# Optimization experiments

Measured on AMD Instinct MI355X. Metric: run time of the kernel, lower is better.

The kernel has to match this reference:

```python
import jax, jax.numpy as jnp
import numpy as np

# Config matching init_kwargs / input shapes
DIM = 96        # dim == C
NH = 6          # num_heads
KS = 7          # kernel_size (local window)
GW = 4          # group_width for the grouped conv in Hadamard-attn branch
B, D, H, W = 2, 8, 96, 96
HD = DIM // NH          # head dim (dim_qk == dim_v == dim)
SCALE = HD ** -0.5      # qk_scale default: head_dim**-0.5
PAD = KS // 2
EPS = 1e-5


def setup_inputs() -> dict:
    key = jax.random.key(0)
    ks = jax.random.split(key, 10)
    s = 0.02
    return {
        "x": jax.random.normal(ks[0], (B, DIM, D, H, W), jnp.float32),
        # pre-norm LayerNorm params
        "ln_g": jnp.ones((DIM,), jnp.float32),
        "ln_b": jnp.zeros((DIM,), jnp.float32),
        # q,k projection (fused 1x1): out = 2*dim_qk
        "w_qk": s * jax.random.normal(ks[1], (2 * DIM, DIM), jnp.float32),
        "b_qk": jnp.zeros((2 * DIM,), jnp.float32),
        # v projection (1x1)
        "w_v": s * jax.random.normal(ks[2], (DIM, DIM), jnp.float32),
        "b_v": jnp.zeros((DIM,), jnp.float32),
        # Hadamard-attention branch: grouped KSxKS conv (groups = DIM//GW)
        "w_a1": s * jax.random.normal(ks[3], (DIM, GW, KS, KS), jnp.float32),
        "b_a1": jnp.zeros((DIM,), jnp.float32),
        # 1x1 conv producing per-head local attention logits (NH * KS^2 channels)
        "w_a2": s * jax.random.normal(ks[4], (NH * KS * KS, DIM), jnp.float32),
        "b_a2": jnp.zeros((NH * KS * KS,), jnp.float32),
        # ghost head (lam=1, gamma=1): attn = h_attn * ghost_mul + ghost_add
        "g_mul": 1.0 + s * jax.random.normal(ks[5], (NH * KS * KS,), jnp.float32),
        "g_add": s * jax.random.normal(ks[6], (NH * KS * KS,), jnp.float32),
        # output projection (1x1)
        "w_p": s * jax.random.normal(ks[7], (DIM, DIM), jnp.float32),
        "b_p": jnp.zeros((DIM,), jnp.float32),
    }


def _elsa_block(x, ln_g, ln_b, w_qk, b_qk, w_v, b_v, w_a1, b_a1, w_a2, b_a2,
                g_mul, g_add, w_p, b_p):
    """x: (Bp, H, W, C) channel-last frames. Pre-norm residual ELSA attention."""
    Bp, Hh, Ww, C = x.shape
    # LayerNorm over channels
    mu = jnp.mean(x, axis=-1, keepdims=True)
    var = jnp.mean(jnp.square(x - mu), axis=-1, keepdims=True)
    xn = (x - mu) * jax.lax.rsqrt(var + EPS) * ln_g + ln_b

    # 1x1 q,k,v projections (channel-last matmuls)
    qk = xn @ w_qk.T + b_qk                      # (Bp,H,W,2C)
    q, k = jnp.split(qk, 2, axis=-1)
    v = xn @ w_v.T + b_v                         # (Bp,H,W,C)

    # Hadamard product -> attention logits via grouped conv + GELU + 1x1
    h = jnp.transpose(q * k * SCALE, (0, 3, 1, 2))   # (Bp,C,H,W) NCHW
    a = jax.lax.conv_general_dilated(
        h, w_a1, window_strides=(1, 1), padding='SAME',
        feature_group_count=C // GW) + b_a1[None, :, None, None]
    a = jax.nn.gelu(a, approximate=False)
    a = jnp.einsum('bchw,oc->bohw', a, w_a2) + b_a2[None, :, None, None]

    # ghost head (lam=1, gamma=1): elementwise scale + static bias per (head, tap)
    attn = a * g_mul[None, :, None, None] + g_add[None, :, None, None]
    attn = attn.reshape(Bp, NH, KS * KS, Hh, Ww)     # (Bp,nh,k^2,H,W)

    # local window aggregation (unfold-free: 49 shifted fused multiply-adds)
    vr = jnp.transpose(v, (0, 3, 1, 2)).reshape(Bp, NH, HD, Hh, Ww)
    vp = jnp.pad(vr, ((0, 0), (0, 0), (0, 0), (PAD, PAD), (PAD, PAD)))
    out = jnp.zeros_like(vr)
    for i in range(KS):
        for j in range(KS):
            out = out + attn[:, :, i * KS + j, None] * vp[:, :, :, i:i + Hh, j:j + Ww]

    out = jnp.transpose(out.reshape(Bp, C, Hh, Ww), (0, 2, 3, 1))  # (Bp,H,W,C)
    y = out @ w_p.T + b_p
    return x + y


def reference(x, ln_g, ln_b, w_qk, b_qk, w_v, b_v, w_a1, b_a1, w_a2, b_a2,
              g_mul, g_add, w_p, b_p):
    b, c, d, hh, ww = x.shape
    # 'b c s h w -> (b s) h w c'
    xf = jnp.transpose(x, (0, 2, 3, 4, 1)).reshape(b * d, hh, ww, c)
    yf = _elsa_block(xf, ln_g, ln_b, w_qk, b_qk, w_v, b_v, w_a1, b_a1,
                     w_a2, b_a2, g_mul, g_add, w_p, b_p)
    # '(b s) h w c -> b c s h w'
    return jnp.transpose(yf.reshape(b, d, hh, ww, c), (0, 4, 1, 2, 3))
```

## Files before the change

### kernel.cpp

```cpp
#include <hip/hip_runtime.h>
#include <hip/hip_bf16.h>


typedef unsigned short u16;
typedef short bf16x8 __attribute__((ext_vector_type(8)));
typedef float floatx4 __attribute__((ext_vector_type(4)));
typedef unsigned short ushort8 __attribute__((ext_vector_type(8)));
typedef unsigned short ushort4v __attribute__((ext_vector_type(4)));
typedef unsigned int uint4v __attribute__((ext_vector_type(4)));
typedef unsigned int uint2v __attribute__((ext_vector_type(2)));
typedef _Float16 f16x2 __attribute__((ext_vector_type(2)));

#define PIX      9216
#define SCALE_QK 0.25f

__device__ __forceinline__ float lo2f(unsigned int u) {
  union { unsigned int i; float f; } z; z.i = u << 16; return z.f;
}
__device__ __forceinline__ float hi2f(unsigned int u) {
  union { unsigned int i; float f; } z; z.i = u & 0xFFFF0000u; return z.f;
}
__device__ __forceinline__ u16 f2b(float f) {
  union { float f; unsigned int i; } z; z.f = f;
  unsigned int r = z.i + 0x7fffu + ((z.i >> 16) & 1u);
  return (u16)(r >> 16);
}
__device__ __forceinline__ u16 f2h(float f) {
  _Float16 h = (_Float16)f;
  union { _Float16 h; u16 u; } z; z.h = h; return z.u;
}
__device__ __forceinline__ f16x2 u2h(unsigned int u) {
  union { unsigned int u; f16x2 h; } z; z.u = u; return z.h;
}
__device__ __forceinline__ float dot2(unsigned int w, unsigned int x, float acc) {
#if __has_builtin(__builtin_amdgcn_fdot2)
  return __builtin_amdgcn_fdot2(u2h(w), u2h(x), acc, false);
#else
  f16x2 a = u2h(w), b = u2h(x);
  return acc + (float)a[0] * (float)b[0] + (float)a[1] * (float)b[1];
#endif
}

__global__ void k_prep(const float* __restrict__ w_qk, const float* __restrict__ b_qk,
                       const float* __restrict__ w_v,  const float* __restrict__ b_v,
                       const float* __restrict__ w_a1,
                       const float* __restrict__ w_a2, const float* __restrict__ b_a2,
                       const float* __restrict__ g_mul,const float* __restrict__ g_add,
                       const float* __restrict__ w_p,  const float* __restrict__ b_p,
                       u16* __restrict__ W2, float* __restrict__ bias2,
                       u16* __restrict__ WA2, float* __restrict__ biasA2,
                       u16* __restrict__ WP, float* __restrict__ biasP,
                       unsigned int* __restrict__ WCV) {
  int i = blockIdx.x * 256 + threadIdx.x;
  if (i < 30720) {
    int r = i / 96, ci = i % 96;
    float val = 0.f;
    if (r < 192) { int src = (r & 1) ? (96 + (r >> 1)) : (r >> 1); val = w_qk[src * 96 + ci]; }
    else if (r < 288) val = w_v[(r - 192) * 96 + ci];
    W2[i] = f2b(val);
  } else if (i < 31040) {
    int r = i - 30720; float bv = 0.f;
    if (r < 192) { int src = (r & 1) ? (96 + (r >> 1)) : (r >> 1); bv = b_qk[src]; }
    else if (r < 288) bv = b_v[r - 192];
    bias2[r] = bv;
  } else if (i < 61760) {
    int j = i - 31040; int r = j / 96, ci = j % 96;
    float wv = 0.f;
    if (r < 294) wv = w_a2[r * 96 + ci] * g_mul[r];
    WA2[j] = f2b(wv);
  } else if (i < 62080) {
    int r = i - 61760; float bv = 0.f;
    if (r < 294) bv = b_a2[r] * g_mul[r] + g_add[r];
    biasA2[r] = bv;
  } else if (i < 74368) {
    int j = i - 62080; int r = j / 96;
    WP[j] = (r < 96) ? f2b(w_p[j]) : (u16)0;
  } else if (i < 74496) {
    int r = i - 74368;
    biasP[r] = (r < 96) ? b_p[r] : 0.f;
  } else if (i < 93312) {
    int j = i - 74496;
    int u = j % 7, co = (j / 7) & 3, ky = (j / 28) % 7, ch = (j / 196) & 3, g = j / 784;
    const float* wsrc = &w_a1[(g * 4 + co) * 196 + ch * 49 + ky * 7];
    float a, b;
    if (u < 3)       { a = wsrc[2 * u];     b = wsrc[2 * u + 1]; }
    else if (u == 3) { a = wsrc[6];         b = 0.f; }
    else             { int t = u - 3;       a = wsrc[2 * t - 1]; b = wsrc[2 * t]; }
    WCV[j] = (unsigned int)f2h(a) | ((unsigned int)f2h(b) << 16);
  }
}

__global__ __launch_bounds__(256) void k_ln(const float* __restrict__ x,
                                            const float* __restrict__ lg,
                                            const float* __restrict__ lb,
                                            u16* __restrict__ xn) {
  int idx = blockIdx.x * 256 + threadIdx.x;
  int f = idx / PIX, p = idx % PIX;
  int b = f >> 3, d = f & 7;
  size_t base = ((size_t)(b * 768 + d)) * PIX + p;
  float s = 0.f, ss = 0.f;
  for (int c = 0; c < 96; ++c) {
    float v = x[base + (size_t)c * 73728];
    s += v; ss += v * v;
  }
  float mu = s * (1.f / 96.f);
  float var = ss * (1.f / 96.f) - mu * mu;
  float rs = rsqrtf(var + 1e-5f);
  size_t ob = (size_t)idx * 96;
  for (int c0 = 0; c0 < 96; c0 += 8) {
    ushort8 pack;
    for (int u = 0; u < 8; ++u) {
      int c = c0 + u;
      float v = x[base + (size_t)c * 73728];
      pack[u] = f2b((v - mu) * rs * lg[c] + lb[c]);
    }
    *(ushort8*)&xn[ob + c0] = pack;
  }
}

template <int MODE>
__global__ __launch_bounds__(256) void k_gemm(const u16* __restrict__ X,
                                              const u16* __restrict__ W,
                                              const float* __restrict__ bias,
                                              u16* __restrict__ out0,
                                              u16* __restrict__ out1,
                                              float* __restrict__ outF,
                                              const float* __restrict__ resid,
                                              int fArg) {
  __shared__ u16 lw[64 * 104];
  __shared__ u16 lx[64 * 104];
  const int tid = threadIdx.x;
  const int fc = blockIdx.z;
  const int f = (MODE == 1) ? (fArg + fc) : fc;
  const int p0 = blockIdx.x * 64;
  const int cot = blockIdx.y;

  if constexpr (MODE == 0) {
    for (int ch = tid; ch < 768; ch += 256) {
      int r = ch / 12, s2 = ch % 12;
      *(uint4v*)&lw[r * 104 + s2 * 8] = *(const uint4v*)&W[(size_t)(cot * 64 + r) * 96 + s2 * 8];
      *(uint4v*)&lx[r * 104 + s2 * 8] = *(const uint4v*)&X[((size_t)(f * PIX + p0 + r)) * 96 + s2 * 8];
    }
  } else {
    for (int ch = tid; ch < 768; ch += 256) {
      int r = ch / 12, s2 = ch % 12;
      *(uint4v*)&lw[r * 104 + s2 * 8] = *(const uint4v*)&W[(size_t)(cot * 64 + r) * 96 + s2 * 8];
    }
    for (int idx = tid; idx < 768; idx += 256) {
      int s2 = idx >> 6, r = idx & 63;
      const u16* src0 = &X[((size_t)(f * 24 + 2 * s2) * PIX + p0 + r) * 4];
      const u16* src1 = &X[((size_t)(f * 24 + 2 * s2 + 1) * PIX + p0 + r) * 4];
      *(uint2v*)&lx[r * 104 + s2 * 8]     = *(const uint2v*)src0;
      *(uint2v*)&lx[r * 104 + s2 * 8 + 4] = *(const uint2v*)src1;
    }
  }
  __syncthreads();

  const int lane = tid & 63, wv = tid >> 6;
  const int cw = (wv >> 1) * 32, pw = (wv & 1) * 32;
  const int m = lane & 15, quad = lane >> 4;

  floatx4 acc[2][2] = {};
  for (int ks = 0; ks < 3; ++ks) {
    int ko = ks * 32 + quad * 8;
    bf16x8 a0 = *(const bf16x8*)&lw[(cw + m) * 104 + ko];
    bf16x8 a1 = *(const bf16x8*)&lw[(cw + 16 + m) * 104 + ko];
    bf16x8 b0 = *(const bf16x8*)&lx[(pw + m) * 104 + ko];
    bf16x8 b1 = *(const bf16x8*)&lx[(pw + 16 + m) * 104 + ko];
    acc[0][0] = __builtin_amdgcn_mfma_f32_16x16x32_bf16(a0, b0, acc[0][0], 0, 0, 0);
    acc[0][1] = __builtin_amdgcn_mfma_f32_16x16x32_bf16(a0, b1, acc[0][1], 0, 0, 0);
    acc[1][0] = __builtin_amdgcn_mfma_f32_16x16x32_bf16(a1, b0, acc[1][0], 0, 0, 0);
    acc[1][1] = __builtin_amdgcn_mfma_f32_16x16x32_bf16(a1, b1, acc[1][1], 0, 0, 0);
  }

  for (int mt = 0; mt < 2; ++mt)
    for (int nt = 0; nt < 2; ++nt) {
      int R = cot * 64 + cw + mt * 16 + quad * 4;
      int pc = p0 + pw + nt * 16 + m;
      floatx4 v4 = acc[mt][nt];
      if (MODE == 0) {
        if (cot < 3) {
          float q0 = v4[0] + bias[R + 0], k0 = v4[1] + bias[R + 1];
          float q1 = v4[2] + bias[R + 2], k1 = v4[3] + bias[R + 3];
          int hc = R >> 1;
          out0[((size_t)f * 96 + hc) * PIX + pc]     = f2h(q0 * k0 * SCALE_QK);
          out0[((size_t)f * 96 + hc + 1) * PIX + pc] = f2h(q1 * k1 * SCALE_QK);
        } else {
          for (int r = 0; r < 4; ++r) {
            int vr = R + r - 192;
            if (vr < 96) out1[((size_t)f * 96 + vr) * PIX + pc] = f2b(v4[r] + bias[R + r]);
          }
        }
      } else if (MODE == 1) {
        for (int r = 0; r < 4; ++r) {
          int o = R + r;
          if (o < 294) out0[((size_t)fc * 294 + o) * PIX + pc] = f2b(v4[r] + bias[o]);
        }
      } else {
        int b = f >> 3, d = f & 7;
        for (int r = 0; r < 4; ++r) {
          int o = R + r;
          if (o < 96) {
            size_t gi = ((size_t)(b * 96 + o) * 8 + d) * PIX + pc;
            outF[gi] = resid[gi] + v4[r] + bias[o];
          }
        }
      }
    }
}

__global__ __launch_bounds__(256, 4) void k_conv(const u16* __restrict__ h,
                                                 const unsigned int* __restrict__ wcv,
                                                 const float* __restrict__ b_a1,
                                                 u16* __restrict__ a_t) {
  __shared__ u16 li[4 * 22 * 104];
  const int g = blockIdx.x, ty = blockIdx.y, f = blockIdx.z;
  const int tid = threadIdx.x;
  const int gb = g * 4, y0 = ty * 16;
  for (int idx = tid; idx < 4576; idx += 256) {
    int row = idx / 52;
    int jd  = idx - row * 52;
    int ch  = row / 22;
    int rr  = row - ch * 22;
    int ay  = y0 - 3 + rr;
    unsigned int val = 0;
    if (jd >= 2 && jd <= 49 && ay >= 0 && ay < 96)
      val = *(const unsigned int*)&h[((size_t)f * 96 + gb + ch) * PIX + ay * 96 + (2 * jd - 4)];
    *(unsigned int*)&li[row * 104 + 2 * jd] = val;
  }
  __syncthreads();

  const int y = tid >> 4;
  const int x0 = (tid & 15) * 6;
  float acc[4][6];
  #pragma unroll
  for (int co = 0; co < 4; ++co) {
    float bv = b_a1[gb + co];
    #pragma unroll
    for (int o = 0; o < 6; ++o) acc[co][o] = bv;
  }

  for (int ch = 0; ch < 4; ++ch)
    for (int ky = 0; ky < 7; ++ky) {
      const unsigned int* wrow = &wcv[(((g * 4 + ch) * 7) + ky) * 28];
      const unsigned int* lsrc =
          (const unsigned int*)&li[(ch * 22 + (y + ky)) * 104 + x0];
      unsigned int IN[7];
      #pragma unroll
      for (int t = 0; t < 7; ++t) IN[t] = lsrc[t];
      #pragma unroll
      for (int co = 0; co < 4; ++co) {
        unsigned int w0 = wrow[co * 7 + 0], w1 = wrow[co * 7 + 1];
        unsigned int w2 = wrow[co * 7 + 2], w3 = wrow[co * 7 + 3];
        unsigned int w4 = wrow[co * 7 + 4], w5 = wrow[co * 7 + 5];
        unsigned int w6 = wrow[co * 7 + 6];
        unsigned int o0 = w0 << 16;
        float a;
        a = acc[co][0]; a = dot2(o0, IN[0], a); a = dot2(w4, IN[1], a);
                        a = dot2(w5, IN[2], a); a = dot2(w6, IN[3], a); acc[co][0] = a;
        a = acc[co][1]; a = dot2(w0, IN[1], a); a = dot2(w1, IN[2], a);
                        a = dot2(w2, IN[3], a); a = dot2(w3, IN[4], a); acc[co][1] = a;
        a = acc[co][2]; a = dot2(o0, IN[1], a); a = dot2(w4, IN[2], a);
                        a = dot2(w5, IN[3], a); a = dot2(w6, IN[4], a); acc[co][2] = a;
        a = acc[co][3]; a = dot2(w0, IN[2], a); a = dot2(w1, IN[3], a);
                        a = dot2(w2, IN[4], a); a = dot2(w3, IN[5], a); acc[co][3] = a;
        a = acc[co][4]; a = dot2(o0, IN[2], a); a = dot2(w4, IN[3], a);
                        a = dot2(w5, IN[4], a); a = dot2(w6, IN[5], a); acc[co][4] = a;
        a = acc[co][5]; a = dot2(w0, IN[3], a); a = dot2(w1, IN[4], a);
                        a = dot2(w2, IN[5], a); a = dot2(w3, IN[6], a); acc[co][5] = a;
      }
    }

  size_t obase = ((size_t)(f * 24 + g) * PIX + (size_t)(y0 + y) * 96 + x0) * 4;
  #pragma unroll
  for (int o = 0; o < 6; o += 2) {
    ushort8 r8;
    #pragma unroll
    for (int co = 0; co < 4; ++co) {
      float a0 = acc[co][o], a1 = acc[co][o + 1];
      r8[co]     = f2b(0.5f * a0 * (1.f + erff(a0 * 0.70710678118f)));
      r8[co + 4] = f2b(0.5f * a1 * (1.f + erff(a1 * 0.70710678118f)));
    }
    *(ushort8*)&a_t[obase + o * 4] = r8;
  }
}

__global__ __launch_bounds__(256, 4) void k_aggr(const u16* __restrict__ attn_c,
                                                 const u16* __restrict__ v,
                                                 u16* __restrict__ out_t,
                                                 int fbase) {
  __shared__ u16 lv[4 * 22 * 104];
  const int wgid = blockIdx.x + 24 * (blockIdx.y + 6 * blockIdx.z);
  const int xcd = wgid & 7;
  const int member = (wgid >> 3) & 3;
  const int slot = wgid >> 5;
  const int gidx = slot * 8 + xcd;
  const int cqh = gidx % 6;
  const int ty = (gidx / 6) % 6;
  const int fc = gidx / 36;
  const int cq = cqh * 4 + member;
  const int f = fbase + fc;
  const int tid = threadIdx.x;
  const int c0 = cq * 4, y0 = ty * 16;
  const int head = c0 >> 4;
  for (int idx = tid; idx < 4 * 22 * 104; idx += 256) {
    int col = idx % 104;
    int rr = (idx / 104) % 22;
    int ch = idx / (104 * 22);
    int ax = col - 3, ay = y0 - 3 + rr;
    u16 val = 0;
    if (ax >= 0 && ax < 96 && ay >= 0 && ay < 96)
      val = v[((size_t)f * 96 + c0 + ch) * PIX + ay * 96 + ax];
    lv[idx] = val;
  }
  __syncthreads();

  const int y = tid >> 4;
  const int x0 = (tid & 15) * 6;
  float acc[4][6] = {};
  const int prow = (y0 + y) * 96 + x0;

  for (int i = 0; i < 7; ++i) {
    float vrow[4][12];
    #pragma unroll
    for (int ch = 0; ch < 4; ++ch) {
      const unsigned int* lsrc = (const unsigned int*)&lv[(ch * 22 + (y + i)) * 104 + x0];
      #pragma unroll
      for (int t = 0; t < 6; ++t) {
        unsigned int u = lsrc[t];
        vrow[ch][2 * t]     = lo2f(u);
        vrow[ch][2 * t + 1] = hi2f(u);
      }
    }
    #pragma unroll
    for (int j = 0; j < 7; ++j) {
      const unsigned int* asrc = (const unsigned int*)
          &attn_c[((size_t)fc * 294 + head * 49 + i * 7 + j) * PIX + prow];
      unsigned int u0 = asrc[0], u1 = asrc[1], u2 = asrc[2];
      float av[6] = {lo2f(u0), hi2f(u0), lo2f(u1), hi2f(u1), lo2f(u2), hi2f(u2)};
      #pragma unroll
      for (int o = 0; o < 6; ++o)
        #pragma unroll
        for (int ch = 0; ch < 4; ++ch)
          acc[ch][o] += av[o] * vrow[ch][o + j];
    }
  }

  size_t obase = ((size_t)(f * 24 + cq) * PIX + prow) * 4;
  #pragma unroll
  for (int o = 0; o < 6; o += 2) {
    ushort8 r8;
    #pragma unroll
    for (int ch = 0; ch < 4; ++ch) {
      r8[ch]     = f2b(acc[ch][o]);
      r8[ch + 4] = f2b(acc[ch][o + 1]);
    }
    *(ushort8*)&out_t[obase + o * 4] = r8;
  }
}

extern "C" void kernel_launch(void* const* d_in, const int* in_sizes, int n_in,
                              void* d_out, int out_size, void* d_ws, size_t ws_size,
                              hipStream_t stream) {
  const float* x    = (const float*)d_in[0];
  const float* ln_g = (const float*)d_in[1];
  const float* ln_b = (const float*)d_in[2];
  const float* w_qk = (const float*)d_in[3];
  const float* b_qk = (const float*)d_in[4];
  const float* w_v  = (const float*)d_in[5];
  const float* b_v  = (const float*)d_in[6];
  const float* w_a1 = (const float*)d_in[7];
  const float* b_a1 = (const float*)d_in[8];
  const float* w_a2 = (const float*)d_in[9];
  const float* b_a2 = (const float*)d_in[10];
  const float* g_mul= (const float*)d_in[11];
  const float* g_add= (const float*)d_in[12];
  const float* w_p  = (const float*)d_in[13];
  const float* b_p  = (const float*)d_in[14];

  char* ws = (char*)d_ws;
  u16*   W2    = (u16*)(ws + 0);
  float* bias2 = (float*)(ws + 61440);
  u16*   WA2   = (u16*)(ws + 62720);
  float* biasA2= (float*)(ws + 124160);
  u16*   WP    = (u16*)(ws + 125440);
  float* biasP = (float*)(ws + 150016);
  unsigned int* WCV = (unsigned int*)(ws + 150528);
  u16*   xn_t  = (u16*)(ws + 225792);
  u16*   hbuf  = (u16*)(ws + 28537344);
  u16*   vbuf  = (u16*)(ws + 56848896);
  u16*   attnc = (u16*)(ws + 85160448);

  k_prep<<<365, 256, 0, stream>>>(w_qk, b_qk, w_v, b_v, w_a1, w_a2, b_a2, g_mul, g_add,
                                  w_p, b_p, W2, bias2, WA2, biasA2, WP, biasP, WCV);
  k_ln<<<576, 256, 0, stream>>>(x, ln_g, ln_b, xn_t);
  k_gemm<0><<<dim3(144, 5, 16), 256, 0, stream>>>(xn_t, W2, bias2, hbuf, vbuf,
                                                  nullptr, nullptr, 0);
  k_conv<<<dim3(24, 6, 16), 256, 0, stream>>>(hbuf, WCV, b_a1, xn_t );
  for (int c = 0; c < 2; ++c) {
    k_gemm<1><<<dim3(144, 5, 8), 256, 0, stream>>>(xn_t , WA2, biasA2,
                                                   attnc, nullptr, nullptr, nullptr, c * 8);
    k_aggr<<<dim3(24, 6, 8), 256, 0, stream>>>(attnc, vbuf, hbuf , c * 8);
  }
  k_gemm<2><<<dim3(144, 2, 16), 256, 0, stream>>>(hbuf , WP, biasP,
                                                  nullptr, nullptr, (float*)d_out, x, 0);
}
```

Baseline: 395.0 us.

## Use packed fp16 FMA for grouped conv and XCD-aware block mapping in GEMMs

The grouped 7x7 conv now keeps fp16x2 accumulators and issues packed FMAs, using alignbit to build odd-offset input pairs instead of dot2 with split weight packing. The weight prep duplicates each tap into both halves, and the bias moves to the epilogue. The GEMM kernels switch to a 1D grid remapped so that the output-tile blocks sharing an input tile land on the same XCD, aiming for better L2 reuse. Accumulating in fp16 instead of fp32 risks precision loss across 196 taps.

Measured after the change: 398.3 us. Within noise of the previous version (+0.8%).

```diff
diff --git a/kernel.cpp b/kernel.cpp
--- a/kernel.cpp
+++ b/kernel.cpp
@@ -6,7 +6,6 @@
 typedef short bf16x8 __attribute__((ext_vector_type(8)));
 typedef float floatx4 __attribute__((ext_vector_type(4)));
 typedef unsigned short ushort8 __attribute__((ext_vector_type(8)));
-typedef unsigned short ushort4v __attribute__((ext_vector_type(4)));
 typedef unsigned int uint4v __attribute__((ext_vector_type(4)));
 typedef unsigned int uint2v __attribute__((ext_vector_type(2)));
 typedef _Float16 f16x2 __attribute__((ext_vector_type(2)));
@@ -29,15 +28,14 @@
   _Float16 h = (_Float16)f;
   union { _Float16 h; u16 u; } z; z.h = h; return z.u;
 }
-__device__ __forceinline__ f16x2 u2h(unsigned int u) {
+__device__ __forceinline__ f16x2 upk(unsigned int u) {
   union { unsigned int u; f16x2 h; } z; z.u = u; return z.h;
 }
-__device__ __forceinline__ float dot2(unsigned int w, unsigned int x, float acc) {
-#if __has_builtin(__builtin_amdgcn_fdot2)
-  return __builtin_amdgcn_fdot2(u2h(w), u2h(x), acc, false);
+__device__ __forceinline__ f16x2 pkfma(unsigned int w, unsigned int x, f16x2 c) {
+#if __has_builtin(__builtin_elementwise_fma)
+  return __builtin_elementwise_fma(upk(w), upk(x), c);
 #else
-  f16x2 a = u2h(w), b = u2h(x);
-  return acc + (float)a[0] * (float)b[0] + (float)a[1] * (float)b[1];
+  return upk(w) * upk(x) + c;
 #endif
 }
 
@@ -80,13 +78,10 @@
     biasP[r] = (r < 96) ? b_p[r] : 0.f;
   } else if (i < 93312) {
     int j = i - 74496;
-    int u = j % 7, co = (j / 7) & 3, ky = (j / 28) % 7, ch = (j / 196) & 3, g = j / 784;
-    const float* wsrc = &w_a1[(g * 4 + co) * 196 + ch * 49 + ky * 7];
-    float a, b;
-    if (u < 3)       { a = wsrc[2 * u];     b = wsrc[2 * u + 1]; }
-    else if (u == 3) { a = wsrc[6];         b = 0.f; }
-    else             { int t = u - 3;       a = wsrc[2 * t - 1]; b = wsrc[2 * t]; }
-    WCV[j] = (unsigned int)f2h(a) | ((unsigned int)f2h(b) << 16);
+    int kx = j % 7, co = (j / 7) & 3, ky = (j / 28) % 7, ch = (j / 196) & 3, g = j / 784;
+    float w = w_a1[(g * 4 + co) * 196 + ch * 49 + ky * 7 + kx];
+    unsigned int hw = f2h(w);
+    WCV[j] = hw | (hw << 16);
   }
 }
 
@@ -129,11 +124,16 @@
                                               int fArg) {
   __shared__ u16 lw[64 * 104];
   __shared__ u16 lx[64 * 104];
+  const int NC = (MODE == 2) ? 2 : 5;
+  const int d = blockIdx.x;
+  const int xcd = d & 7, idx0 = d >> 3;
+  const int cot = idx0 % NC, fi = idx0 / NC;
+  const int fam = fi * 8 + xcd;
+  const int pt = fam % 144;
+  const int fc = fam / 144;
+  const int f = (MODE == 1) ? (fArg + fc) : fc;
+  const int p0 = pt * 64;
   const int tid = threadIdx.x;
-  const int fc = blockIdx.z;
-  const int f = (MODE == 1) ? (fArg + fc) : fc;
-  const int p0 = blockIdx.x * 64;
-  const int cot = blockIdx.y;
 
   if constexpr (MODE == 0) {
     for (int ch = tid; ch < 768; ch += 256) {
@@ -197,11 +197,11 @@
           if (o < 294) out0[((size_t)fc * 294 + o) * PIX + pc] = f2b(v4[r] + bias[o]);
         }
       } else {
-        int b = f >> 3, d = f & 7;
+        int b = f >> 3, dd = f & 7;
         for (int r = 0; r < 4; ++r) {
           int o = R + r;
           if (o < 96) {
-            size_t gi = ((size_t)(b * 96 + o) * 8 + d) * PIX + pc;
+            size_t gi = ((size_t)(b * 96 + o) * 8 + dd) * PIX + pc;
             outF[gi] = resid[gi] + v4[r] + bias[o];
           }
         }
@@ -232,56 +232,63 @@
 
   const int y = tid >> 4;
   const int x0 = (tid & 15) * 6;
-  float acc[4][6];
+  f16x2 pacc[4][3];
   #pragma unroll
-  for (int co = 0; co < 4; ++co) {
-    float bv = b_a1[gb + co];
+  for (int co = 0; co < 4; ++co)
     #pragma unroll
-    for (int o = 0; o < 6; ++o) acc[co][o] = bv;
-  }
-
-  for (int ch = 0; ch < 4; ++ch)
+    for (int p = 0; p < 3; ++p) pacc[co][p] = upk(0u);
+
+  for (int ch = 0; ch < 4; ++ch) {
+    const unsigned int* wch = &wcv[784 * g + 196 * ch];
     for (int ky = 0; ky < 7; ++ky) {
-      const unsigned int* wrow = &wcv[(((g * 4 + ch) * 7) + ky) * 28];
       const unsigned int* lsrc =
           (const unsigned int*)&li[(ch * 22 + (y + ky)) * 104 + x0];
-      unsigned int IN[7];
-      #pragma unroll
-      for (int t = 0; t < 7; ++t) IN[t] = lsrc[t];
+      unsigned int D0 = lsrc[0], D1 = lsrc[1], D2 = lsrc[2], D3 = lsrc[3];
+      unsigned int D4 = lsrc[4], D5 = lsrc[5], D6 = lsrc[6];
+      unsigned int S0 = __builtin_amdgcn_alignbit(D1, D0, 16);
+      unsigned int S1 = __builtin_amdgcn_alignbit(D2, D1, 16);
+      unsigned int S2 = __builtin_amdgcn_alignbit(D3, D2, 16);
+      unsigned int S3 = __builtin_amdgcn_alignbit(D4, D3, 16);
+      unsigned int S4 = __builtin_amdgcn_alignbit(D5, D4, 16);
+      unsigned int S5 = __builtin_amdgcn_alignbit(D6, D5, 16);
+      const unsigned int* wb = wch + 28 * ky;
       #pragma unroll
       for (int co = 0; co < 4; ++co) {
-        unsigned int w0 = wrow[co * 7 + 0], w1 = wrow[co * 7 + 1];
-        unsigned int w2 = wrow[co * 7 + 2], w3 = wrow[co * 7 + 3];
-        unsigned int w4 = wrow[co * 7 + 4], w5 = wrow[co * 7 + 5];
-        unsigned int w6 = wrow[co * 7 + 6];
-        unsigned int o0 = w0 << 16;
-        float a;
-        a = acc[co][0]; a = dot2(o0, IN[0], a); a = dot2(w4, IN[1], a);
-                        a = dot2(w5, IN[2], a); a = dot2(w6, IN[3], a); acc[co][0] = a;
-        a = acc[co][1]; a = dot2(w0, IN[1], a); a = dot2(w1, IN[2], a);
-                        a = dot2(w2, IN[3], a); a = dot2(w3, IN[4], a); acc[co][1] = a;
-        a = acc[co][2]; a = dot2(o0, IN[1], a); a = dot2(w4, IN[2], a);
-                        a = dot2(w5, IN[3], a); a = dot2(w6, IN[4], a); acc[co][2] = a;
-        a = acc[co][3]; a = dot2(w0, IN[2], a); a = dot2(w1, IN[3], a);
-                        a = dot2(w2, IN[4], a); a = dot2(w3, IN[5], a); acc[co][3] = a;
-        a = acc[co][4]; a = dot2(o0, IN[2], a); a = dot2(w4, IN[3], a);
-                        a = dot2(w5, IN[4], a); a = dot2(w6, IN[5], a); acc[co][4] = a;
-        a = acc[co][5]; a = dot2(w0, IN[3], a); a = dot2(w1, IN[4], a);
-                        a = dot2(w2, IN[5], a); a = dot2(w3, IN[6], a); acc[co][5] = a;
+        unsigned int w0 = wb[co * 7 + 0], w1 = wb[co * 7 + 1];
+        unsigned int w2 = wb[co * 7 + 2], w3 = wb[co * 7 + 3];
+        unsigned int w4 = wb[co * 7 + 4], w5 = wb[co * 7 + 5];
+        unsigned int w6 = wb[co * 7 + 6];
+        f16x2 a;
+        a = pacc[co][0];
+        a = pkfma(w0, S0, a); a = pkfma(w1, D1, a); a = pkfma(w2, S1, a);
+        a = pkfma(w3, D2, a); a = pkfma(w4, S2, a); a = pkfma(w5, D3, a);
+        a = pkfma(w6, S3, a); pacc[co][0] = a;
+        a = pacc[co][1];
+        a = pkfma(w0, S1, a); a = pkfma(w1, D2, a); a = pkfma(w2, S2, a);
+        a = pkfma(w3, D3, a); a = pkfma(w4, S3, a); a = pkfma(w5, D4, a);
+        a = pkfma(w6, S4, a); pacc[co][1] = a;
+        a = pacc[co][2];
+        a = pkfma(w0, S2, a); a = pkfma(w1, D3, a); a = pkfma(w2, S3, a);
+        a = pkfma(w3, D4, a); a = pkfma(w4, S4, a); a = pkfma(w5, D5, a);
+        a = pkfma(w6, S5, a); pacc[co][2] = a;
       }
     }
+  }
 
   size_t obase = ((size_t)(f * 24 + g) * PIX + (size_t)(y0 + y) * 96 + x0) * 4;
+  float bv0 = b_a1[gb + 0], bv1 = b_a1[gb + 1], bv2 = b_a1[gb + 2], bv3 = b_a1[gb + 3];
   #pragma unroll
-  for (int o = 0; o < 6; o += 2) {
+  for (int p = 0; p < 3; ++p) {
     ushort8 r8;
     #pragma unroll
     for (int co = 0; co < 4; ++co) {
-      float a0 = acc[co][o], a1 = acc[co][o + 1];
+      float bv = (co == 0) ? bv0 : (co == 1) ? bv1 : (co == 2) ? bv2 : bv3;
+      f16x2 v = pacc[co][p];
+      float a0 = (float)v[0] + bv, a1 = (float)v[1] + bv;
       r8[co]     = f2b(0.5f * a0 * (1.f + erff(a0 * 0.70710678118f)));
       r8[co + 4] = f2b(0.5f * a1 * (1.f + erff(a1 * 0.70710678118f)));
     }
-    *(ushort8*)&a_t[obase + o * 4] = r8;
+    *(ushort8*)&a_t[obase + p * 8] = r8;
   }
 }
 
@@ -394,14 +401,14 @@
   k_prep<<<365, 256, 0, stream>>>(w_qk, b_qk, w_v, b_v, w_a1, w_a2, b_a2, g_mul, g_add,
                                   w_p, b_p, W2, bias2, WA2, biasA2, WP, biasP, WCV);
   k_ln<<<576, 256, 0, stream>>>(x, ln_g, ln_b, xn_t);
-  k_gemm<0><<<dim3(144, 5, 16), 256, 0, stream>>>(xn_t, W2, bias2, hbuf, vbuf,
-                                                  nullptr, nullptr, 0);
+  k_gemm<0><<<144 * 5 * 16, 256, 0, stream>>>(xn_t, W2, bias2, hbuf, vbuf,
+                                              nullptr, nullptr, 0);
   k_conv<<<dim3(24, 6, 16), 256, 0, stream>>>(hbuf, WCV, b_a1, xn_t );
   for (int c = 0; c < 2; ++c) {
-    k_gemm<1><<<dim3(144, 5, 8), 256, 0, stream>>>(xn_t , WA2, biasA2,
-                                                   attnc, nullptr, nullptr, nullptr, c * 8);
+    k_gemm<1><<<144 * 5 * 8, 256, 0, stream>>>(xn_t , WA2, biasA2,
+                                               attnc, nullptr, nullptr, nullptr, c * 8);
     k_aggr<<<dim3(24, 6, 8), 256, 0, stream>>>(attnc, vbuf, hbuf , c * 8);
   }
-  k_gemm<2><<<dim3(144, 2, 16), 256, 0, stream>>>(hbuf , WP, biasP,
-                                                  nullptr, nullptr, (float*)d_out, x, 0);
-}
+  k_gemm<2><<<144 * 2 * 16, 256, 0, stream>>>(hbuf , WP, biasP,
+                                              nullptr, nullptr, (float*)d_out, x, 0);
+}
```
